# Kernel tuning notes

Hardware: AMD Instinct MI355X
Metric: run time of the kernel (lower is better)

## Reference

```python
import jax, jax.numpy as jnp
import numpy as np

K = 3       # kernel_size
RATE = 2    # dilation rate
NH = 8      # num_heads
EPS = 1e-5  # InstanceNorm eps


def _conv1x1(x, W, b):
    # x: [B,C,H,W], W: [O,C], b: [O]
    return jnp.einsum('bchw,oc->bohw', x, W) + b[None, :, None, None]


def _inorm(x):
    mu = jnp.mean(x, axis=(2, 3), keepdims=True)
    var = jnp.var(x, axis=(2, 3), keepdims=True)
    return (x - mu) / jnp.sqrt(var + EPS)


def _extract_patches(x):
    # dilated KxK patches, stride 1, 'same' grid -> [B, C, K*K, H, W]
    B, C, H, W = x.shape
    pad = RATE * (K - 1) // 2
    xp = jnp.pad(x, ((0, 0), (0, 0), (pad, pad), (pad, pad)))
    taps = [xp[:, :, i * RATE:i * RATE + H, j * RATE:j * RATE + W]
            for i in range(K) for j in range(K)]
    return jnp.stack(taps, axis=2)


def setup_inputs() -> dict:
    key = jax.random.key(0)
    ks = jax.random.split(key, 8)
    B, C, H, W, A = 1, 64, 64, 64, 128
    features = jax.random.normal(ks[0], (B, C, H, W), jnp.float32)
    masks = jax.random.uniform(ks[1], (B, 1, H, W), jnp.float32)
    s_in = 1.0 / np.sqrt(C).astype(np.float32)
    Wq = jax.random.normal(ks[2], (A, C), jnp.float32) * s_in
    bq = jnp.zeros((A,), jnp.float32)
    Wk = jax.random.normal(ks[3], (A, C), jnp.float32) * s_in
    bk = jnp.zeros((A,), jnp.float32)
    Wo = jax.random.normal(ks[4], (C, C), jnp.float32) * s_in
    bo = jnp.zeros((C,), jnp.float32)
    return dict(features=features, masks=masks, Wq=Wq, bq=bq,
                Wk=Wk, bk=bk, Wo=Wo, bo=bo)


def reference(features, masks, Wq, bq, Wk, bk, Wo, bo):
    B, C, H, W = features.shape
    A = Wq.shape[0]
    hc = A // NH
    L = H * W
    KK = K * K

    m = (masks > 0.5).astype(features.dtype)          # 1 = hole
    f_masked = features * m
    f_unmasked = features * (1.0 - m)

    q = jax.nn.relu(_inorm(_conv1x1(f_masked, Wq, bq)))    # [B,A,H,W]
    k = jax.nn.relu(_inorm(_conv1x1(f_unmasked, Wk, bk)))  # [B,A,H,W]

    # per-head dilated patch banks: [B,NH,hc*KK,L]
    qp = _extract_patches(q).reshape(B, NH, hc * KK, L)
    kp = _extract_patches(k).reshape(B, NH, hc * KK, L)

    # patch-correlation attention per head: [B,NH,L,L]
    attn = jax.nn.softmax(jnp.einsum('bndq,bndk->bnqk', qp, kp), axis=-1)

    # value patch bank from unmasked features: [B,C*KK,L]
    vp = _extract_patches(f_unmasked).reshape(B, C * KK, L)

    # sample value patches: [B,NH,L,C*KK]
    sampled = jnp.einsum('bnqk,bdk->bnqd', attn, vp)

    # fold: average the KK taps per channel, then average over heads
    attended = sampled.reshape(B, NH, L, C, KK).mean(axis=4).mean(axis=1)  # [B,L,C]
    attended = attended.transpose(0, 2, 1).reshape(B, C, H, W)

    return jax.nn.relu(_inorm(_conv1x1(attended, Wo, bo)))
```

## Files before the change

### kernel.cpp

```cpp
#include <hip/hip_runtime.h>
#include <hip/hip_bf16.h>


#define LL 4096
#define CC 64
#define AA 128
#define NH_ 8
#define KSTR 168
#define VSTR 72
#define LOG2E 1.44269504088896340736f

typedef _Float16 half8 __attribute__((ext_vector_type(8)));
typedef float floatx4 __attribute__((ext_vector_type(4)));

__device__ __forceinline__ float fexp2(float x) {
    float r;
    asm("v_exp_f32 %0, %1" : "=v"(r) : "v"(x));
    return r;
}

__global__ __launch_bounds__(256) void prep_kernel(
    const float* __restrict__ feat,
    const float* __restrict__ masks,
    const float* __restrict__ Wq, const float* __restrict__ bq,
    const float* __restrict__ Wk, const float* __restrict__ bk,
    _Float16* __restrict__ q_act, _Float16* __restrict__ k_act,
    _Float16* __restrict__ vb)
{
    const int tid = threadIdx.x;
    const int b = blockIdx.x;
    __shared__ float sW[CC];
    __shared__ float sm[8];

    if (b >= 2 * AA) {
        int c = b - 2 * AA;
        for (int p = 0; p < 16; ++p) {
            int l = p * 256 + tid;
            int y = l >> 6, x = l & 63;
            float s = 0.f;
            for (int ty = 0; ty < 3; ++ty) {
                int yy = y + 2 * (ty - 1);
                if (yy < 0 || yy > 63) continue;
                for (int tx = 0; tx < 3; ++tx) {
                    int xx = x + 2 * (tx - 1);
                    if (xx < 0 || xx > 63) continue;
                    int ll = yy * 64 + xx;
                    float hole = masks[ll] > 0.5f ? 1.f : 0.f;
                    s += feat[c * LL + ll] * (1.f - hole);
                }
            }
            vb[c * LL + l] = (_Float16)(s * (1.f / 9.f));
        }
        return;
    }

    const int a = b & (AA - 1);
    const int sel = b >> 7;
    const float* Wrow = (sel ? Wk : Wq) + a * CC;
    const float bias = sel ? bk[a] : bq[a];
    if (tid < CC) sW[tid] = Wrow[tid];
    __syncthreads();

    float acc[16];
#pragma unroll
    for (int p = 0; p < 16; ++p) acc[p] = 0.f;
    for (int c = 0; c < CC; ++c) {
        float wc = sW[c];
        const float* fr = feat + (size_t)c * LL + tid;
#pragma unroll
        for (int p = 0; p < 16; ++p) acc[p] += wc * fr[p * 256];
    }

    float vals[16];
    float s1 = 0.f, s2 = 0.f;
#pragma unroll
    for (int p = 0; p < 16; ++p) {
        int l = p * 256 + tid;
        float hole = masks[l] > 0.5f ? 1.f : 0.f;
        float mf = sel ? (1.f - hole) : hole;
        float v = acc[p] * mf + bias;
        vals[p] = v; s1 += v; s2 += v * v;
    }
    for (int off = 32; off; off >>= 1) {
        s1 += __shfl_down(s1, off, 64);
        s2 += __shfl_down(s2, off, 64);
    }
    int wv = tid >> 6, ln = tid & 63;
    if (ln == 0) { sm[wv * 2] = s1; sm[wv * 2 + 1] = s2; }
    __syncthreads();
    s1 = sm[0] + sm[2] + sm[4] + sm[6];
    s2 = sm[1] + sm[3] + sm[5] + sm[7];
    float mu = s1 * (1.f / LL);
    float inv = rsqrtf(s2 * (1.f / LL) - mu * mu + 1e-5f);

    const float oscale = sel ? 1.f : LOG2E;
    _Float16* act = (sel ? k_act : q_act) + (size_t)a * LL;
#pragma unroll
    for (int p = 0; p < 16; ++p) {
        int l = p * 256 + tid;
        float v = (vals[p] - mu) * inv;
        act[l] = (_Float16)(v > 0.f ? v * oscale : 0.f);
    }
}

__global__ __launch_bounds__(256) void build_kp(
    const _Float16* __restrict__ k_act, _Float16* __restrict__ kp)
{
    const int n = blockIdx.x, y = blockIdx.y;
    const int tid = threadIdx.x;
    const _Float16* ka = k_act + (size_t)n * 16 * LL;
    _Float16* base = kp + ((size_t)n * LL + y * 64) * KSTR;
#pragma unroll
    for (int i = 0; i < 6; ++i) {
        int idx = tid + i * 256;
        if (idx >= 64 * 21) break;
        int x = idx / 21, c21 = idx - x * 21;
        half8 v8;
#pragma unroll
        for (int j = 0; j < 8; ++j) {
            int d = c21 * 8 + j;
            _Float16 v = (_Float16)0.f;
            if (d < 144) {
                int ah = d / 9, t = d - ah * 9;
                int ty = t / 3, tx = t - ty * 3;
                int yy = y + 2 * (ty - 1);
                int xx = x + 2 * (tx - 1);
                if (yy >= 0 && yy <= 63 && xx >= 0 && xx <= 63)
                    v = ka[ah * LL + yy * 64 + xx];
            }
            v8[j] = v;
        }
        *(half8*)(base + (size_t)idx * 8) = v8;
    }
}

__global__ __launch_bounds__(256, 2) void attn_kernel(
    const _Float16* __restrict__ q_act, const _Float16* __restrict__ kp,
    const _Float16* __restrict__ vb,
    _Float16* __restrict__ Opart, float* __restrict__ ml)
{
    const int qt2 = blockIdx.x, n = blockIdx.y, h = blockIdx.z;
    const int jt0 = h * 32;
    const int tid = threadIdx.x;
    const int w = tid >> 6, lane = tid & 63;
    const int l15 = lane & 15, quad = lane >> 4;

    __shared__ __align__(16) _Float16 Bk[2][64 * KSTR];
    __shared__ __align__(16) _Float16 Vt[2][64 * VSTR];
    __shared__ __align__(16) _Float16 Pb[4][2][16 * VSTR];

    const _Float16* kpn = kp + (size_t)n * LL * KSTR;
    const uint4* vbu = (const uint4*)vb;

    const int vc0 = tid >> 3, ve0 = tid & 7;
    const int vc1 = (tid + 256) >> 3, ve1 = tid & 7;

    auto issue_bk = [&](int jt, _Float16* dst) {
        const char* tile = (const char*)(kpn + (size_t)jt * 64 * KSTR) + (lane << 4);
        for (int c = w; c < 21; c += 4) {
            __builtin_amdgcn_global_load_lds(
                (const __attribute__((address_space(1))) void*)(tile + c * 1024),
                (__attribute__((address_space(3))) void*)(dst + c * 512),
                16, 0, 0);
        }
    };

    half8 afrag[2][5];
    {
        const _Float16* qa = q_act + (size_t)n * 16 * LL;
        const int x = w * 16 + l15;
#pragma unroll
        for (int rs = 0; rs < 2; ++rs) {
            const int y = qt2 * 2 + rs;
#pragma unroll
            for (int ks = 0; ks < 5; ++ks) {
#pragma unroll
                for (int j = 0; j < 8; ++j) {
                    int d = ks * 32 + quad * 8 + j;
                    _Float16 v = (_Float16)0.f;
                    if (d < 144) {
                        int ah = d / 9, t = d - ah * 9;
                        int ty = t / 3, tx = t - ty * 3;
                        int yy = y + 2 * (ty - 1);
                        int xx = x + 2 * (tx - 1);
                        if (yy >= 0 && yy <= 63 && xx >= 0 && xx <= 63)
                            v = qa[ah * LL + yy * 64 + xx];
                    }
                    afrag[rs][ks][j] = v;
                }
            }
        }
    }

    floatx4 accO[2][4];
    float mrow[2][4], lrow[2][4];
#pragma unroll
    for (int rs = 0; rs < 2; ++rs)
#pragma unroll
        for (int i = 0; i < 4; ++i) {
            accO[rs][i] = (floatx4){0.f, 0.f, 0.f, 0.f};
            mrow[rs][i] = -1e30f; lrow[rs][i] = 0.f;
        }

    uint4 vreg[2];
    issue_bk(jt0, Bk[0]);
    vreg[0] = vbu[vc0 * (LL / 8) + jt0 * 8 + ve0];
    vreg[1] = vbu[vc1 * (LL / 8) + jt0 * 8 + ve1];

    int cur = 0;
    for (int it = 0; it < 32; ++it) {
        {
            uint4* vd = (uint4*)Vt[cur];
            vd[vc0 * 9 + ve0] = vreg[0];
            vd[vc1 * 9 + ve1] = vreg[1];
        }

        __syncthreads();

        if (it < 31) {
            const int jn = jt0 + it + 1;
            issue_bk(jn, Bk[cur ^ 1]);
            vreg[0] = vbu[vc0 * (LL / 8) + jn * 8 + ve0];
            vreg[1] = vbu[vc1 * (LL / 8) + jn * 8 + ve1];
        }

        const _Float16* bk = Bk[cur];
        const _Float16* vt = Vt[cur];

        floatx4 accS[2][4];
#pragma unroll
        for (int rs = 0; rs < 2; ++rs)
#pragma unroll
            for (int i = 0; i < 4; ++i) accS[rs][i] = (floatx4){0.f, 0.f, 0.f, 0.f};
        __builtin_amdgcn_s_setprio(1);
        for (int ks = 0; ks < 5; ++ks) {
#pragma unroll
            for (int nt = 0; nt < 4; ++nt) {
                half8 bfr = *(const half8*)(bk + (nt * 16 + l15) * KSTR + ks * 32 + quad * 8);
                accS[0][nt] = __builtin_amdgcn_mfma_f32_16x16x32_f16(afrag[0][ks], bfr, accS[0][nt], 0, 0, 0);
                accS[1][nt] = __builtin_amdgcn_mfma_f32_16x16x32_f16(afrag[1][ks], bfr, accS[1][nt], 0, 0, 0);
            }
        }
        __builtin_amdgcn_s_setprio(0);

#pragma unroll
        for (int rs = 0; rs < 2; ++rs) {
#pragma unroll
            for (int r = 0; r < 4; ++r) {
                float tm = fmaxf(fmaxf(accS[rs][0][r], accS[rs][1][r]),
                                 fmaxf(accS[rs][2][r], accS[rs][3][r]));
                if (!__all(tm <= mrow[rs][r] + 3.0f)) {
#pragma unroll
                    for (int off = 8; off; off >>= 1) tm = fmaxf(tm, __shfl_xor(tm, off, 16));
                    float mn = fmaxf(mrow[rs][r], tm);
                    float alpha = fexp2(mrow[rs][r] - mn);
                    mrow[rs][r] = mn;
                    lrow[rs][r] *= alpha;
#pragma unroll
                    for (int nt = 0; nt < 4; ++nt) accO[rs][nt][r] *= alpha;
                }
                float rsum = 0.f;
#pragma unroll
                for (int nt = 0; nt < 4; ++nt) {
                    float pv = fexp2(accS[rs][nt][r] - mrow[rs][r]);
                    accS[rs][nt][r] = pv;
                    rsum += pv;
                }
                lrow[rs][r] += rsum;
            }

            _Float16* pw = Pb[w][rs];
#pragma unroll
            for (int nt = 0; nt < 4; ++nt)
#pragma unroll
                for (int r = 0; r < 4; ++r)
                    pw[(quad * 4 + r) * VSTR + ((nt ^ quad) << 4) + l15] = (_Float16)accS[rs][nt][r];
        }

        __builtin_amdgcn_s_setprio(1);
#pragma unroll
        for (int ks = 0; ks < 2; ++ks) {
            int kb = ks * 2 + (quad >> 1);
            const int poff = l15 * VSTR + ((kb ^ (l15 >> 2)) << 4) + (quad & 1) * 8;
            half8 afr0 = *(const half8*)(Pb[w][0] + poff);
            half8 afr1 = *(const half8*)(Pb[w][1] + poff);
#pragma unroll
            for (int nt = 0; nt < 4; ++nt) {
                half8 bfr = *(const half8*)(vt + (nt * 16 + l15) * VSTR + ks * 32 + quad * 8);
                accO[0][nt] = __builtin_amdgcn_mfma_f32_16x16x32_f16(afr0, bfr, accO[0][nt], 0, 0, 0);
                accO[1][nt] = __builtin_amdgcn_mfma_f32_16x16x32_f16(afr1, bfr, accO[1][nt], 0, 0, 0);
            }
        }
        __builtin_amdgcn_s_setprio(0);

        cur ^= 1;
    }

#pragma unroll
    for (int rs = 0; rs < 2; ++rs) {
        const int y = qt2 * 2 + rs;
#pragma unroll
        for (int r = 0; r < 4; ++r) {
            float rsum = lrow[rs][r];
#pragma unroll
            for (int off = 8; off; off >>= 1) rsum += __shfl_xor(rsum, off, 16);
            lrow[rs][r] = rsum;
        }

        _Float16* op = Opart + ((size_t)(n * 2 + h) * LL + y * 64 + w * 16) * CC;
#pragma unroll
        for (int r = 0; r < 4; ++r) {
            float invl = 1.f / lrow[rs][r];
            int row = quad * 4 + r;
#pragma unroll
            for (int nt = 0; nt < 4; ++nt)
                op[row * CC + nt * 16 + l15] = (_Float16)(accO[rs][nt][r] * invl);
            if (l15 == 0) {
                float* mlp = ml + ((size_t)n * LL + y * 64 + w * 16 + row) * 4;
                mlp[2 * h] = mrow[rs][r];
                mlp[2 * h + 1] = lrow[rs][r];
            }
        }
    }
}

__global__ __launch_bounds__(256) void combine_kernel(
    const _Float16* __restrict__ Opart, const float* __restrict__ ml,
    float* __restrict__ att)
{
    int t = blockIdx.x * 256 + threadIdx.x;
    int l = t >> 6, c = t & 63;
    float s = 0.f;
#pragma unroll
    for (int n = 0; n < NH_; ++n) {
        const float* mlp = ml + ((size_t)n * LL + l) * 4;
        float m0 = mlp[0], l0 = mlp[1], m1 = mlp[2], l1 = mlp[3];
        float M = fmaxf(m0, m1);
        float w0 = l0 * fexp2(m0 - M);
        float w1 = l1 * fexp2(m1 - M);
        float o0 = (float)Opart[((size_t)(2 * n) * LL + l) * CC + c];
        float o1 = (float)Opart[((size_t)(2 * n + 1) * LL + l) * CC + c];
        s += (w0 * o0 + w1 * o1) / (w0 + w1);
    }
    att[t] = s * 0.125f;
}

__global__ __launch_bounds__(256) void out_kernel(
    const float* __restrict__ att,
    const float* __restrict__ Wo, const float* __restrict__ bo,
    float* __restrict__ out)
{
    const int o = blockIdx.x;
    const int tid = threadIdx.x;
    __shared__ float sW[CC];
    __shared__ float sm[8];
    if (tid < CC) sW[tid] = Wo[o * CC + tid];
    __syncthreads();
    const float bias = bo[o];

    float vals[16], s1 = 0.f, s2 = 0.f;
    for (int p = 0; p < 16; ++p) {
        int l = p * 256 + tid;
        const float4* arow = (const float4*)(att + (size_t)l * CC);
        float acc = bias;
#pragma unroll
        for (int c4 = 0; c4 < 16; ++c4) {
            float4 a4 = arow[c4];
            acc += sW[c4 * 4] * a4.x + sW[c4 * 4 + 1] * a4.y +
                   sW[c4 * 4 + 2] * a4.z + sW[c4 * 4 + 3] * a4.w;
        }
        vals[p] = acc; s1 += acc; s2 += acc * acc;
    }
    for (int off = 32; off; off >>= 1) {
        s1 += __shfl_down(s1, off, 64);
        s2 += __shfl_down(s2, off, 64);
    }
    int wv = tid >> 6, ln = tid & 63;
    if (ln == 0) { sm[wv * 2] = s1; sm[wv * 2 + 1] = s2; }
    __syncthreads();
    s1 = sm[0] + sm[2] + sm[4] + sm[6];
    s2 = sm[1] + sm[3] + sm[5] + sm[7];
    float mu = s1 * (1.f / LL);
    float inv = rsqrtf(s2 * (1.f / LL) - mu * mu + 1e-5f);
    for (int p = 0; p < 16; ++p) {
        int l = p * 256 + tid;
        float v = (vals[p] - mu) * inv;
        out[(size_t)o * LL + l] = v > 0.f ? v : 0.f;
    }
}

extern "C" void kernel_launch(void* const* d_in, const int* in_sizes, int n_in,
                              void* d_out, int out_size, void* d_ws, size_t ws_size,
                              hipStream_t stream) {
    const float* feat  = (const float*)d_in[0];
    const float* masks = (const float*)d_in[1];
    const float* Wq    = (const float*)d_in[2];
    const float* bq    = (const float*)d_in[3];
    const float* Wk    = (const float*)d_in[4];
    const float* bk    = (const float*)d_in[5];
    const float* Wo    = (const float*)d_in[6];
    const float* bo    = (const float*)d_in[7];
    float* out = (float*)d_out;

    char* ws = (char*)d_ws;
    _Float16* q_act = (_Float16*)ws;
    _Float16* k_act = (_Float16*)(ws + 1048576);
    _Float16* vb    = (_Float16*)(ws + 2097152);
    float*    att   = (float*)(ws + 2621440);
    _Float16* kp    = (_Float16*)(ws + 3670016);
    _Float16* Opart = (_Float16*)(ws + 14680064);
    float*    ml    = (float*)(ws + 23068672);

    prep_kernel<<<2 * AA + CC, 256, 0, stream>>>(feat, masks, Wq, bq, Wk, bk,
                                                 q_act, k_act, vb);
    dim3 gb(NH_, 64);
    build_kp<<<gb, 256, 0, stream>>>(k_act, kp);
    dim3 g(32, NH_, 2);
    attn_kernel<<<g, 256, 0, stream>>>(q_act, kp, vb, Opart, ml);
    combine_kernel<<<LL * CC / 256, 256, 0, stream>>>(Opart, ml, att);
    out_kernel<<<CC, 256, 0, stream>>>(att, Wo, bo, out);
}
```

Measured before the change: 245.8 us.

## Transpose QK MFMA and pass P to PV via bpermute instead of LDS

Swaps the operand order of the QK^T MFMA so each lane holds scores for one query row across columns, which makes the softmax max and sum a 4-lane cross-quad reduction rather than per-row 16-lane shuffles. The probabilities are packed to fp16 and moved into A-fragment layout with ds_bpermute, removing the per-wave LDS staging buffer Pb and its stores and loads. The K patch bank stride also drops from 168 to 144 halfs, so less padding is loaded. V tiles now use an XOR-swizzled unpadded layout. In exchange the kernel adds bpermute and select instructions, and with the unpadded K stride the B-fragment LDS reads may hit more bank conflicts.

```diff
diff --git a/kernel.cpp b/kernel.cpp
--- a/kernel.cpp
+++ b/kernel.cpp
@@ -6,12 +6,12 @@
 #define CC 64
 #define AA 128
 #define NH_ 8
-#define KSTR 168
-#define VSTR 72
+#define KSTR 144
 #define LOG2E 1.44269504088896340736f
 
 typedef _Float16 half8 __attribute__((ext_vector_type(8)));
 typedef float floatx4 __attribute__((ext_vector_type(4)));
+typedef int intx4 __attribute__((ext_vector_type(4)));
 
 __device__ __forceinline__ float fexp2(float x) {
     float r;
@@ -111,26 +111,25 @@
     const _Float16* ka = k_act + (size_t)n * 16 * LL;
     _Float16* base = kp + ((size_t)n * LL + y * 64) * KSTR;
 #pragma unroll
-    for (int i = 0; i < 6; ++i) {
+    for (int i = 0; i < 5; ++i) {
         int idx = tid + i * 256;
-        if (idx >= 64 * 21) break;
-        int x = idx / 21, c21 = idx - x * 21;
-        half8 v8;
-#pragma unroll
-        for (int j = 0; j < 8; ++j) {
-            int d = c21 * 8 + j;
-            _Float16 v = (_Float16)0.f;
-            if (d < 144) {
+        if (idx < 64 * 18) {
+            int x = idx / 18, c18 = idx - x * 18;
+            half8 v8;
+#pragma unroll
+            for (int j = 0; j < 8; ++j) {
+                int d = c18 * 8 + j;
                 int ah = d / 9, t = d - ah * 9;
                 int ty = t / 3, tx = t - ty * 3;
                 int yy = y + 2 * (ty - 1);
                 int xx = x + 2 * (tx - 1);
+                _Float16 v = (_Float16)0.f;
                 if (yy >= 0 && yy <= 63 && xx >= 0 && xx <= 63)
                     v = ka[ah * LL + yy * 64 + xx];
-            }
-            v8[j] = v;
-        }
-        *(half8*)(base + (size_t)idx * 8) = v8;
+                v8[j] = v;
+            }
+            *(half8*)(base + (size_t)idx * 8) = v8;
+        }
     }
 }
 
@@ -145,19 +144,22 @@
     const int w = tid >> 6, lane = tid & 63;
     const int l15 = lane & 15, quad = lane >> 4;
 
-    __shared__ __align__(16) _Float16 Bk[2][64 * KSTR];
-    __shared__ __align__(16) _Float16 Vt[2][64 * VSTR];
-    __shared__ __align__(16) _Float16 Pb[4][2][16 * VSTR];
+    __shared__ __align__(16) _Float16 Bk[2][64 * KSTR + 16];
+    __shared__ __align__(16) _Float16 Vt[2][64 * 64];
+
+    if (tid < 32) Bk[tid >> 4][64 * KSTR + (tid & 15)] = (_Float16)0.f;
 
     const _Float16* kpn = kp + (size_t)n * LL * KSTR;
     const uint4* vbu = (const uint4*)vb;
 
     const int vc0 = tid >> 3, ve0 = tid & 7;
-    const int vc1 = (tid + 256) >> 3, ve1 = tid & 7;
+    const int vc1 = vc0 + 32, ve1 = ve0;
+    const int vs0 = vc0 * 8 + (ve0 ^ (vc0 & 7));
+    const int vs1 = vc1 * 8 + (ve1 ^ (vc1 & 7));
 
     auto issue_bk = [&](int jt, _Float16* dst) {
         const char* tile = (const char*)(kpn + (size_t)jt * 64 * KSTR) + (lane << 4);
-        for (int c = w; c < 21; c += 4) {
+        for (int c = w; c < 18; c += 4) {
             __builtin_amdgcn_global_load_lds(
                 (const __attribute__((address_space(1))) void*)(tile + c * 1024),
                 (__attribute__((address_space(3))) void*)(dst + c * 512),
@@ -193,14 +195,17 @@
     }
 
     floatx4 accO[2][4];
-    float mrow[2][4], lrow[2][4];
-#pragma unroll
-    for (int rs = 0; rs < 2; ++rs)
-#pragma unroll
-        for (int i = 0; i < 4; ++i) {
-            accO[rs][i] = (floatx4){0.f, 0.f, 0.f, 0.f};
-            mrow[rs][i] = -1e30f; lrow[rs][i] = 0.f;
-        }
+    float mrow[2], lrow[2];
+#pragma unroll
+    for (int rs = 0; rs < 2; ++rs) {
+        mrow[rs] = -1e30f; lrow[rs] = 0.f;
+#pragma unroll
+        for (int i = 0; i < 4; ++i) accO[rs][i] = (floatx4){0.f, 0.f, 0.f, 0.f};
+    }
+
+    const int aLo = (((quad & 1) << 5) + l15) << 2;
+    const int aHi = aLo + 64;
+    const bool selHi = (quad >> 1) != 0;
 
     uint4 vreg[2];
     issue_bk(jt0, Bk[0]);
@@ -211,8 +216,8 @@
     for (int it = 0; it < 32; ++it) {
         {
             uint4* vd = (uint4*)Vt[cur];
-            vd[vc0 * 9 + ve0] = vreg[0];
-            vd[vc1 * 9 + ve1] = vreg[1];
+            vd[vs0] = vreg[0];
+            vd[vs1] = vreg[1];
         }
 
         __syncthreads();
@@ -237,58 +242,83 @@
 #pragma unroll
             for (int nt = 0; nt < 4; ++nt) {
                 half8 bfr = *(const half8*)(bk + (nt * 16 + l15) * KSTR + ks * 32 + quad * 8);
-                accS[0][nt] = __builtin_amdgcn_mfma_f32_16x16x32_f16(afrag[0][ks], bfr, accS[0][nt], 0, 0, 0);
-                accS[1][nt] = __builtin_amdgcn_mfma_f32_16x16x32_f16(afrag[1][ks], bfr, accS[1][nt], 0, 0, 0);
+                accS[0][nt] = __builtin_amdgcn_mfma_f32_16x16x32_f16(bfr, afrag[0][ks], accS[0][nt], 0, 0, 0);
+                accS[1][nt] = __builtin_amdgcn_mfma_f32_16x16x32_f16(bfr, afrag[1][ks], accS[1][nt], 0, 0, 0);
             }
         }
         __builtin_amdgcn_s_setprio(0);
 
+        half8 pfr[2][2];
 #pragma unroll
         for (int rs = 0; rs < 2; ++rs) {
-#pragma unroll
-            for (int r = 0; r < 4; ++r) {
-                float tm = fmaxf(fmaxf(accS[rs][0][r], accS[rs][1][r]),
-                                 fmaxf(accS[rs][2][r], accS[rs][3][r]));
-                if (!__all(tm <= mrow[rs][r] + 3.0f)) {
-#pragma unroll
-                    for (int off = 8; off; off >>= 1) tm = fmaxf(tm, __shfl_xor(tm, off, 16));
-                    float mn = fmaxf(mrow[rs][r], tm);
-                    float alpha = fexp2(mrow[rs][r] - mn);
-                    mrow[rs][r] = mn;
-                    lrow[rs][r] *= alpha;
-#pragma unroll
-                    for (int nt = 0; nt < 4; ++nt) accO[rs][nt][r] *= alpha;
-                }
-                float rsum = 0.f;
-#pragma unroll
-                for (int nt = 0; nt < 4; ++nt) {
-                    float pv = fexp2(accS[rs][nt][r] - mrow[rs][r]);
+            float t0 = fmaxf(fmaxf(accS[rs][0][0], accS[rs][0][1]), fmaxf(accS[rs][0][2], accS[rs][0][3]));
+            float t1 = fmaxf(fmaxf(accS[rs][1][0], accS[rs][1][1]), fmaxf(accS[rs][1][2], accS[rs][1][3]));
+            float t2 = fmaxf(fmaxf(accS[rs][2][0], accS[rs][2][1]), fmaxf(accS[rs][2][2], accS[rs][2][3]));
+            float t3 = fmaxf(fmaxf(accS[rs][3][0], accS[rs][3][1]), fmaxf(accS[rs][3][2], accS[rs][3][3]));
+            float tm = fmaxf(fmaxf(t0, t1), fmaxf(t2, t3));
+            if (!__all(tm <= mrow[rs] + 3.0f)) {
+                tm = fmaxf(tm, __shfl_xor(tm, 16, 64));
+                tm = fmaxf(tm, __shfl_xor(tm, 32, 64));
+                float mn = fmaxf(mrow[rs], tm);
+                float alpha = fexp2(mrow[rs] - mn);
+                mrow[rs] = mn;
+                lrow[rs] *= alpha;
+                float af[4];
+#pragma unroll
+                for (int r = 0; r < 4; ++r) af[r] = __shfl(alpha, quad * 4 + r, 16);
+#pragma unroll
+                for (int nt = 0; nt < 4; ++nt)
+#pragma unroll
+                    for (int r = 0; r < 4; ++r) accO[rs][nt][r] *= af[r];
+            }
+            float rsum = 0.f;
+#pragma unroll
+            for (int nt = 0; nt < 4; ++nt)
+#pragma unroll
+                for (int r = 0; r < 4; ++r) {
+                    float pv = fexp2(accS[rs][nt][r] - mrow[rs]);
                     accS[rs][nt][r] = pv;
                     rsum += pv;
                 }
-                lrow[rs][r] += rsum;
-            }
-
-            _Float16* pw = Pb[w][rs];
+            lrow[rs] += rsum;
+
+            int pkw[4][2];
 #pragma unroll
             for (int nt = 0; nt < 4; ++nt)
 #pragma unroll
-                for (int r = 0; r < 4; ++r)
-                    pw[(quad * 4 + r) * VSTR + ((nt ^ quad) << 4) + l15] = (_Float16)accS[rs][nt][r];
+                for (int rp = 0; rp < 2; ++rp) {
+                    auto hp = __builtin_amdgcn_cvt_pkrtz(accS[rs][nt][2 * rp],
+                                                         accS[rs][nt][2 * rp + 1]);
+                    pkw[nt][rp] = __builtin_bit_cast(int, hp);
+                }
+#pragma unroll
+            for (int ks2 = 0; ks2 < 2; ++ks2) {
+                int w0A = __builtin_amdgcn_ds_bpermute(aLo, pkw[2 * ks2][0]);
+                int w0B = __builtin_amdgcn_ds_bpermute(aLo, pkw[2 * ks2 + 1][0]);
+                int w1A = __builtin_amdgcn_ds_bpermute(aLo, pkw[2 * ks2][1]);
+                int w1B = __builtin_amdgcn_ds_bpermute(aLo, pkw[2 * ks2 + 1][1]);
+                int w2A = __builtin_amdgcn_ds_bpermute(aHi, pkw[2 * ks2][0]);
+                int w2B = __builtin_amdgcn_ds_bpermute(aHi, pkw[2 * ks2 + 1][0]);
+                int w3A = __builtin_amdgcn_ds_bpermute(aHi, pkw[2 * ks2][1]);
+                int w3B = __builtin_amdgcn_ds_bpermute(aHi, pkw[2 * ks2 + 1][1]);
+                intx4 wvv;
+                wvv[0] = selHi ? w0B : w0A;
+                wvv[1] = selHi ? w1B : w1A;
+                wvv[2] = selHi ? w2B : w2A;
+                wvv[3] = selHi ? w3B : w3A;
+                pfr[rs][ks2] = __builtin_bit_cast(half8, wvv);
+            }
         }
 
         __builtin_amdgcn_s_setprio(1);
 #pragma unroll
-        for (int ks = 0; ks < 2; ++ks) {
-            int kb = ks * 2 + (quad >> 1);
-            const int poff = l15 * VSTR + ((kb ^ (l15 >> 2)) << 4) + (quad & 1) * 8;
-            half8 afr0 = *(const half8*)(Pb[w][0] + poff);
-            half8 afr1 = *(const half8*)(Pb[w][1] + poff);
+        for (int ks2 = 0; ks2 < 2; ++ks2) {
 #pragma unroll
             for (int nt = 0; nt < 4; ++nt) {
-                half8 bfr = *(const half8*)(vt + (nt * 16 + l15) * VSTR + ks * 32 + quad * 8);
-                accO[0][nt] = __builtin_amdgcn_mfma_f32_16x16x32_f16(afr0, bfr, accO[0][nt], 0, 0, 0);
-                accO[1][nt] = __builtin_amdgcn_mfma_f32_16x16x32_f16(afr1, bfr, accO[1][nt], 0, 0, 0);
+                half8 bfr = *(const half8*)(vt + (nt * 16 + l15) * 64 +
+                                            (((ks2 * 4 + quad) ^ (l15 & 7)) << 3));
+                accO[0][nt] = __builtin_amdgcn_mfma_f32_16x16x32_f16(pfr[0][ks2], bfr, accO[0][nt], 0, 0, 0);
+                accO[1][nt] = __builtin_amdgcn_mfma_f32_16x16x32_f16(pfr[1][ks2], bfr, accO[1][nt], 0, 0, 0);
             }
         }
         __builtin_amdgcn_s_setprio(0);
@@ -299,27 +329,25 @@
 #pragma unroll
     for (int rs = 0; rs < 2; ++rs) {
         const int y = qt2 * 2 + rs;
-#pragma unroll
-        for (int r = 0; r < 4; ++r) {
-            float rsum = lrow[rs][r];
-#pragma unroll
-            for (int off = 8; off; off >>= 1) rsum += __shfl_xor(rsum, off, 16);
-            lrow[rs][r] = rsum;
-        }
+        float rsum = lrow[rs];
+        rsum += __shfl_xor(rsum, 16, 64);
+        rsum += __shfl_xor(rsum, 32, 64);
+        float invl = 1.f / rsum;
+        float iv[4];
+#pragma unroll
+        for (int r = 0; r < 4; ++r) iv[r] = __shfl(invl, quad * 4 + r, 16);
 
         _Float16* op = Opart + ((size_t)(n * 2 + h) * LL + y * 64 + w * 16) * CC;
 #pragma unroll
-        for (int r = 0; r < 4; ++r) {
-            float invl = 1.f / lrow[rs][r];
-            int row = quad * 4 + r;
+        for (int r = 0; r < 4; ++r)
 #pragma unroll
             for (int nt = 0; nt < 4; ++nt)
-                op[row * CC + nt * 16 + l15] = (_Float16)(accO[rs][nt][r] * invl);
-            if (l15 == 0) {
-                float* mlp = ml + ((size_t)n * LL + y * 64 + w * 16 + row) * 4;
-                mlp[2 * h] = mrow[rs][r];
-                mlp[2 * h + 1] = lrow[rs][r];
-            }
+                op[(quad * 4 + r) * CC + nt * 16 + l15] = (_Float16)(accO[rs][nt][r] * iv[r]);
+
+        if (quad == 0) {
+            float* mlp = ml + ((size_t)n * LL + y * 64 + w * 16 + l15) * 4;
+            mlp[2 * h] = mrow[rs];
+            mlp[2 * h + 1] = rsum;
         }
     }
 }
@@ -408,8 +436,8 @@
     _Float16* vb    = (_Float16*)(ws + 2097152);
     float*    att   = (float*)(ws + 2621440);
     _Float16* kp    = (_Float16*)(ws + 3670016);
-    _Float16* Opart = (_Float16*)(ws + 14680064);
-    float*    ml    = (float*)(ws + 23068672);
+    _Float16* Opart = (_Float16*)(ws + 13107200);
+    float*    ml    = (float*)(ws + 21495808);
 
     prep_kernel<<<2 * AA + CC, 256, 0, stream>>>(feat, masks, Wq, bq, Wk, bk,
                                                  q_act, k_act, vb);
```

New measurement: 232.4 us. 1.06x faster.
